# Performance work log

Hardware: AMD Instinct MI355X
Metric: run time of the kernel (lower is better)

## Reference

```python
import jax, jax.numpy as jnp
import numpy as np

N_NODES = 100000
N_EDGES = 1000000
IN_FEAT = 128
OUT_FEAT = 128
NUM_RELS = 64
NUM_BASES = 16
SUBMAT_IN = IN_FEAT // NUM_BASES   # 8
SUBMAT_OUT = OUT_FEAT // NUM_BASES # 8


def setup_inputs() -> dict:
    key = jax.random.key(0)
    k = jax.random.split(key, 8)
    h = jax.random.normal(k[0], (N_NODES, IN_FEAT), dtype=jnp.float32)
    norm = jax.random.uniform(k[1], (N_EDGES, 1), dtype=jnp.float32)
    src = jax.random.randint(k[2], (N_EDGES,), 0, N_NODES, dtype=jnp.int32)
    dst = jax.random.randint(k[3], (N_EDGES,), 0, N_NODES, dtype=jnp.int32)
    r = jax.random.randint(k[4], (N_EDGES,), 0, NUM_RELS, dtype=jnp.int32)
    # learned params (xavier-uniform style scale)
    wscale = np.sqrt(6.0 / (SUBMAT_IN + SUBMAT_OUT)) * np.sqrt(2.0)
    weight = jax.random.uniform(k[5], (NUM_RELS, NUM_BASES * SUBMAT_IN * SUBMAT_OUT),
                                minval=-wscale, maxval=wscale, dtype=jnp.float32)
    lscale = np.sqrt(6.0 / (IN_FEAT + OUT_FEAT)) * np.sqrt(2.0)
    loop_weight = jax.random.uniform(k[6], (IN_FEAT, OUT_FEAT),
                                     minval=-lscale, maxval=lscale, dtype=jnp.float32)
    h_bias = jnp.zeros((OUT_FEAT,), dtype=jnp.float32)
    return {"h": h, "norm": norm, "weight": weight, "loop_weight": loop_weight,
            "h_bias": h_bias, "src": src, "dst": dst, "r": r}


def reference(h, norm, weight, loop_weight, h_bias, src, dst, r):
    E = src.shape[0]
    # per-edge block-diagonal weights: (E, B, si, so)
    w = weight[r].reshape(E, NUM_BASES, SUBMAT_IN, SUBMAT_OUT)
    # src features split into blocks: (E, B, si)
    hs = h[src].reshape(E, NUM_BASES, SUBMAT_IN)
    # small bmm per block, flatten to (E, OUT_FEAT)
    msg = jnp.einsum('ebi,ebio->ebo', hs, w).reshape(E, OUT_FEAT)
    msg = msg * norm
    # scatter-sum to destination nodes
    agg = jax.ops.segment_sum(msg, dst, num_segments=N_NODES)
    # self-loop message (dropout=0.0) + bias
    out = agg + h_bias + h @ loop_weight
    return jax.nn.relu(out)
```

## Files before the change

### kernel.cpp

```cpp
#include <hip/hip_runtime.h>
#include <stdint.h>

#define N_NODES 100000
#define N_EDGES 1000000
#define IN_F 128
#define OUT_F 128
#define NUM_RELS 64
#define NB_SCAN ((N_NODES + 255) / 256)
#define N_WAVES 16384
#define GEMM_B ((N_NODES + 127) / 128)
#define GATHER_B 256

typedef _Float16 half2v __attribute__((ext_vector_type(2)));

__device__ __forceinline__ float dot2f(uint32_t hu, uint32_t wu, float acc) {
#if __has_builtin(__builtin_amdgcn_fdot2)
    return __builtin_amdgcn_fdot2(__builtin_bit_cast(half2v, hu),
                                  __builtin_bit_cast(half2v, wu), acc, false);
#else
    half2v a = __builtin_bit_cast(half2v, hu);
    half2v b = __builtin_bit_cast(half2v, wu);
    acc = fmaf((float)a.x, (float)b.x, acc);
    acc = fmaf((float)a.y, (float)b.y, acc);
    return acc;
#endif
}

__device__ __forceinline__ uint32_t pkh2(float x, float y) {
    half2v v;
    v.x = (_Float16)x;
    v.y = (_Float16)y;
    return __builtin_bit_cast(uint32_t, v);
}

__global__ __launch_bounds__(256) void prep_gemm_fused(
    const float* __restrict__ h, const float* __restrict__ W,
    const float* __restrict__ bias, float* __restrict__ out,
    const float* __restrict__ weight, uint32_t* __restrict__ wsw,
    const int* __restrict__ dst, int* __restrict__ cnt,
    uint4* __restrict__ h16_4, int n_edges, int do_h16)
{
    if (blockIdx.x < GEMM_B) {
        const int tid = threadIdx.x;
        const int ty = tid >> 4, tx = tid & 15;
        const int node0 = blockIdx.x * 128 + ty * 8;
        const int o0 = tx * 8;

        float acc[8][8];
#pragma unroll
        for (int j = 0; j < 8; ++j)
#pragma unroll
            for (int i = 0; i < 8; ++i) acc[j][i] = 0.f;

        int nidx[8];
#pragma unroll
        for (int j = 0; j < 8; ++j) {
            int n = node0 + j;
            nidx[j] = n < N_NODES ? n : (N_NODES - 1);
        }

        for (int k = 0; k < IN_F; k += 4) {
            float hsv[8][4];
#pragma unroll
            for (int j = 0; j < 8; ++j) {
                float4 hv = *reinterpret_cast<const float4*>(h + (size_t)nidx[j] * IN_F + k);
                *reinterpret_cast<float4*>(hsv[j]) = hv;
            }
#pragma unroll
            for (int kk = 0; kk < 4; ++kk) {
                const float* wrow = W + (size_t)(k + kk) * OUT_F + o0;
                float wr[8];
                *reinterpret_cast<float4*>(wr)     = *reinterpret_cast<const float4*>(wrow);
                *reinterpret_cast<float4*>(wr + 4) = *reinterpret_cast<const float4*>(wrow + 4);
#pragma unroll
                for (int j = 0; j < 8; ++j) {
                    const float hk = hsv[j][kk];
#pragma unroll
                    for (int i = 0; i < 8; ++i)
                        acc[j][i] = fmaf(hk, wr[i], acc[j][i]);
                }
            }
        }

        float br[8];
        *reinterpret_cast<float4*>(br)     = *reinterpret_cast<const float4*>(bias + o0);
        *reinterpret_cast<float4*>(br + 4) = *reinterpret_cast<const float4*>(bias + o0 + 4);

#pragma unroll
        for (int j = 0; j < 8; ++j) {
            int n = node0 + j;
            if (n < N_NODES) {
                float4 v0, v1;
                v0.x = acc[j][0] + br[0]; v0.y = acc[j][1] + br[1];
                v0.z = acc[j][2] + br[2]; v0.w = acc[j][3] + br[3];
                v1.x = acc[j][4] + br[4]; v1.y = acc[j][5] + br[5];
                v1.z = acc[j][6] + br[6]; v1.w = acc[j][7] + br[7];
                float* op = out + (size_t)n * OUT_F + o0;
                *reinterpret_cast<float4*>(op)     = v0;
                *reinterpret_cast<float4*>(op + 4) = v1;
            }
        }
        return;
    }

    int t = (blockIdx.x - GEMM_B) * 256 + threadIdx.x;
    if (t < NUM_RELS * 512) {
        int r    = t >> 9;
        int p    = t & 511;
        int half = p >> 8;
        int w8   = p & 255;
        int l    = w8 >> 2;
        int ip   = w8 & 3;
        int b    = l >> 2;
        int q    = l & 3;
        int o    = 2 * q + half;
        const float* s = weight + (size_t)r * 1024 + b * 64 + (2 * ip) * 8 + o;
        half2v v;
        v.x = (_Float16)s[0];
        v.y = (_Float16)s[8];
        wsw[t] = __builtin_bit_cast(uint32_t, v);
        return;
    }
    int e = t - NUM_RELS * 512;
    if (e < n_edges) {
        atomicAdd(&cnt[dst[e]], 1);
        return;
    }
    if (!do_h16) return;
    int t2 = e - n_edges;
    if (t2 < N_NODES * IN_F / 8) {
        const float4* hp = reinterpret_cast<const float4*>(h + (size_t)t2 * 8);
        float4 a = hp[0], c = hp[1];
        uint4 r;
        r.x = pkh2(a.x, a.y);
        r.y = pkh2(a.z, a.w);
        r.z = pkh2(c.x, c.y);
        r.w = pkh2(c.z, c.w);
        h16_4[t2] = r;
    }
}

__global__ __launch_bounds__(256) void block_sums(
    const int* __restrict__ cnt, int* __restrict__ part, int n)
{
    __shared__ int sdata[256];
    int i = blockIdx.x * 256 + threadIdx.x;
    sdata[threadIdx.x] = (i < n) ? cnt[i] : 0;
    __syncthreads();
    for (int s = 128; s > 0; s >>= 1) {
        if (threadIdx.x < s) sdata[threadIdx.x] += sdata[threadIdx.x + s];
        __syncthreads();
    }
    if (threadIdx.x == 0) part[blockIdx.x] = sdata[0];
}

__global__ __launch_bounds__(256) void write_off2(
    const int* __restrict__ cnt, const int* __restrict__ part,
    int* __restrict__ off, int* __restrict__ cur, int n, int n_edges)
{
    __shared__ int sdata[256];
    __shared__ int buf[256];
    const int tid = threadIdx.x;
    const int bid = blockIdx.x;

    int psum = 0;
    for (int t = tid; t < bid; t += 256) psum += part[t];
    sdata[tid] = psum;
    __syncthreads();
    for (int s = 128; s > 0; s >>= 1) {
        if (tid < s) sdata[tid] += sdata[tid + s];
        __syncthreads();
    }
    const int blockoff = sdata[0];

    int i = bid * 256 + tid;
    int v = (i < n) ? cnt[i] : 0;
    buf[tid] = v;
    __syncthreads();
    for (int ofs = 1; ofs < 256; ofs <<= 1) {
        int t = (tid >= ofs) ? buf[tid - ofs] : 0;
        __syncthreads();
        buf[tid] += t;
        __syncthreads();
    }
    int excl = buf[tid] - v + blockoff;
    if (i < n) { off[i] = excl; cur[i] = excl; }
    if (i == n - 1) off[n] = n_edges;
}

__global__ __launch_bounds__(256) void fill_and_part(
    const int* __restrict__ src, const int* __restrict__ dst,
    const int* __restrict__ rel, const float* __restrict__ norm,
    int* __restrict__ cur, int2* __restrict__ emeta,
    const int* __restrict__ off, int* __restrict__ wstart, int n_edges)
{
    int t = blockIdx.x * 256 + threadIdx.x;
    if (t < n_edges) {
        int d = dst[t];
        int p = atomicAdd(&cur[d], 1);
        int2 m;
        m.x = src[t] | (rel[t] << 20);
        m.y = __float_as_int(norm[t]);
        emeta[p] = m;
    } else {
        int w = t - n_edges;
        if (w <= N_WAVES) {
            if (w == 0) {
                wstart[0] = 0;
            } else if (w == N_WAVES) {
                wstart[N_WAVES] = N_NODES;
            } else {
                int target = (int)(((long long)N_EDGES * w) / N_WAVES);
                int lo = 0, hi = N_NODES - 1;
                while (lo < hi) {
                    int mid = (lo + hi) >> 1;
                    if (off[mid + 1] > target) hi = mid; else lo = mid + 1;
                }
                wstart[w] = lo;
            }
        } else if (w <= N_WAVES + 3) {
            int2 z; z.x = 0; z.y = 0;
            emeta[n_edges + (w - N_WAVES - 1)] = z;
        }
    }
}

__global__ __launch_bounds__(1024, 4) void gather_nodes10(
    const uint4* __restrict__ h16_4, const uint32_t* __restrict__ wsw,
    const int* __restrict__ off, const int2* __restrict__ emeta,
    const int* __restrict__ wstart, float* __restrict__ out)
{
    __shared__ uint32_t wlds[NUM_RELS * 512];

    {
        uint4* l4 = reinterpret_cast<uint4*>(wlds);
        const uint4* g4 = reinterpret_cast<const uint4*>(wsw);
        int t = threadIdx.x;
#pragma unroll
        for (int k = 0; k < 8; ++k)
            l4[t + k * 1024] = g4[t + k * 1024];
    }
    __syncthreads();

    const int lane = threadIdx.x & 63;
    const int wid  = threadIdx.x >> 6;
    const int b = lane >> 2;
    const int q = lane & 3;
    const uint32_t lbase = (uint32_t)(lane * 4);

    for (int wv = blockIdx.x * 16 + wid; wv < N_WAVES; wv += GATHER_B * 16) {
        const int n0 = wstart[wv];
        const int n1 = wstart[wv + 1];
        if (n0 >= n1) continue;

        int j = off[n0];
        int e_next = off[n0 + 1];

        int2 m0 = emeta[j];
        int2 m1 = emeta[j + 1];
        int2 m2 = emeta[j + 2];
        uint4 hv0 = h16_4[((uint32_t)m0.x & 0xFFFFFu) * 16 + b];
        uint4 hv1 = h16_4[((uint32_t)m1.x & 0xFFFFFu) * 16 + b];

        uint32_t base0 = ((uint32_t)m0.x >> 20) * 512 + lbase;
        uint4 wa = *reinterpret_cast<const uint4*>(&wlds[base0]);
        uint4 wb = *reinterpret_cast<const uint4*>(&wlds[base0 + 256]);

        for (int d = n0; d < n1; ++d) {
            const int idx2 = (d + 2 < n1) ? d + 2 : n1;
            const int e_nn = off[idx2];
            float a0 = 0.f, a1 = 0.f;

            while (j < e_next) {
                int2 m3 = emeta[j + 3];
                uint4 hv2 = h16_4[((uint32_t)m2.x & 0xFFFFFu) * 16 + b];
                uint32_t bn = ((uint32_t)m1.x >> 20) * 512 + lbase;
                uint4 wna = *reinterpret_cast<const uint4*>(&wlds[bn]);
                uint4 wnb = *reinterpret_cast<const uint4*>(&wlds[bn + 256]);

                float s0 = dot2f(hv0.x, wa.x, 0.f);
                s0 = dot2f(hv0.y, wa.y, s0);
                s0 = dot2f(hv0.z, wa.z, s0);
                s0 = dot2f(hv0.w, wa.w, s0);
                float s1 = dot2f(hv0.x, wb.x, 0.f);
                s1 = dot2f(hv0.y, wb.y, s1);
                s1 = dot2f(hv0.z, wb.z, s1);
                s1 = dot2f(hv0.w, wb.w, s1);

                const float nm = __int_as_float(m0.y);
                a0 = fmaf(s0, nm, a0);
                a1 = fmaf(s1, nm, a1);

                m0 = m1; m1 = m2; m2 = m3;
                hv0 = hv1; hv1 = hv2;
                wa = wna; wb = wnb;
                ++j;
            }

            float2* op = reinterpret_cast<float2*>(out + (size_t)d * OUT_F + b * 8 + 2 * q);
            float2 bse = *op;
            float2 res;
            res.x = fmaxf(bse.x + a0, 0.f);
            res.y = fmaxf(bse.y + a1, 0.f);
            *op = res;

            e_next = e_nn;
        }
    }
}

__global__ __launch_bounds__(1024, 4) void gather_nodes6(
    const float* __restrict__ h, const uint32_t* __restrict__ wsw,
    const int* __restrict__ off, const int2* __restrict__ emeta,
    const int* __restrict__ wstart, float* __restrict__ out)
{
    __shared__ uint32_t wlds[NUM_RELS * 512];
    {
        uint4* l4 = reinterpret_cast<uint4*>(wlds);
        const uint4* g4 = reinterpret_cast<const uint4*>(wsw);
        int t = threadIdx.x;
#pragma unroll
        for (int k = 0; k < 8; ++k)
            l4[t + k * 1024] = g4[t + k * 1024];
    }
    __syncthreads();

    const int lane = threadIdx.x & 63;
    const int wid  = threadIdx.x >> 6;
    const int b = lane >> 2;
    const int q = lane & 3;
    const uint32_t lbase = (uint32_t)(lane * 4);

    for (int wv = blockIdx.x * 16 + wid; wv < N_WAVES; wv += GATHER_B * 16) {
        const int n0 = wstart[wv];
        const int n1 = wstart[wv + 1];
        if (n0 >= n1) continue;

        int j = off[n0];
        int2 m0 = emeta[j];
        int2 m1 = emeta[j + 1];
        int2 m2 = emeta[j + 2];

        const float4* hr0 = reinterpret_cast<const float4*>(
            h + (size_t)((uint32_t)m0.x & 0xFFFFFu) * IN_F + b * 8);
        float4 h0A = hr0[0], h0B = hr0[1];
        const float4* hr1 = reinterpret_cast<const float4*>(
            h + (size_t)((uint32_t)m1.x & 0xFFFFFu) * IN_F + b * 8);
        float4 h1A = hr1[0], h1B = hr1[1];

        uint32_t base0 = ((uint32_t)m0.x >> 20) * 512 + lbase;
        uint4 wa = *reinterpret_cast<const uint4*>(&wlds[base0]);
        uint4 wb = *reinterpret_cast<const uint4*>(&wlds[base0 + 256]);

        for (int d = n0; d < n1; ++d) {
            const int end_d = off[d + 1];
            float a0 = 0.f, a1 = 0.f;

            while (j < end_d) {
                int2 m3 = emeta[j + 3];
                const float4* hr2 = reinterpret_cast<const float4*>(
                    h + (size_t)((uint32_t)m2.x & 0xFFFFFu) * IN_F + b * 8);
                float4 h2A = hr2[0], h2B = hr2[1];
                uint32_t bn = ((uint32_t)m1.x >> 20) * 512 + lbase;
                uint4 wna = *reinterpret_cast<const uint4*>(&wlds[bn]);
                uint4 wnb = *reinterpret_cast<const uint4*>(&wlds[bn + 256]);

                uint32_t h01 = __builtin_bit_cast(uint32_t, __builtin_amdgcn_cvt_pkrtz(h0A.x, h0A.y));
                uint32_t h23 = __builtin_bit_cast(uint32_t, __builtin_amdgcn_cvt_pkrtz(h0A.z, h0A.w));
                uint32_t h45 = __builtin_bit_cast(uint32_t, __builtin_amdgcn_cvt_pkrtz(h0B.x, h0B.y));
                uint32_t h67 = __builtin_bit_cast(uint32_t, __builtin_amdgcn_cvt_pkrtz(h0B.z, h0B.w));

                float s0 = dot2f(h01, wa.x, 0.f);
                s0 = dot2f(h23, wa.y, s0);
                s0 = dot2f(h45, wa.z, s0);
                s0 = dot2f(h67, wa.w, s0);
                float s1 = dot2f(h01, wb.x, 0.f);
                s1 = dot2f(h23, wb.y, s1);
                s1 = dot2f(h45, wb.z, s1);
                s1 = dot2f(h67, wb.w, s1);

                const float nm = __int_as_float(m0.y);
                a0 = fmaf(s0, nm, a0);
                a1 = fmaf(s1, nm, a1);

                m0 = m1; m1 = m2; m2 = m3;
                h0A = h1A; h0B = h1B; h1A = h2A; h1B = h2B;
                wa = wna; wb = wnb;
                ++j;
            }

            float2* op = reinterpret_cast<float2*>(out + (size_t)d * OUT_F + b * 8 + 2 * q);
            float2 bse = *op;
            float2 res;
            res.x = fmaxf(bse.x + a0, 0.f);
            res.y = fmaxf(bse.y + a1, 0.f);
            *op = res;
        }
    }
}

extern "C" void kernel_launch(void* const* d_in, const int* in_sizes, int n_in,
                              void* d_out, int out_size, void* d_ws, size_t ws_size,
                              hipStream_t stream)
{
    const float* h      = (const float*)d_in[0];
    const float* norm   = (const float*)d_in[1];
    const float* weight = (const float*)d_in[2];
    const float* loop_w = (const float*)d_in[3];
    const float* bias   = (const float*)d_in[4];
    const int*   src    = (const int*)d_in[5];
    const int*   dst    = (const int*)d_in[6];
    const int*   rel    = (const int*)d_in[7];
    float* out = (float*)d_out;

    char* wsb = (char*)d_ws;
    char* ws0 = wsb;
    int*  cnt    = (int*)wsb;  wsb += sizeof(int) * N_NODES;
    int*  off    = (int*)wsb;  wsb += sizeof(int) * (N_NODES + 1);
    int*  cur    = (int*)wsb;  wsb += sizeof(int) * N_NODES;
    int*  part   = (int*)wsb;  wsb += sizeof(int) * 512;
    int*  wstart = (int*)wsb;  wsb += sizeof(int) * (N_WAVES + 1);
    wsb = (char*)(((uintptr_t)wsb + 15) & ~(uintptr_t)15);
    uint32_t* wsw = (uint32_t*)wsb; wsb += sizeof(uint32_t) * NUM_RELS * 512;
    int2* emeta = (int2*)wsb;  wsb += sizeof(int2) * (N_EDGES + 3);
    wsb = (char*)(((uintptr_t)wsb + 15) & ~(uintptr_t)15);
    uint4* h16_4 = (uint4*)wsb; wsb += (size_t)N_NODES * IN_F * 2;

    const int use_h16 = (size_t)(wsb - ws0) <= ws_size;

    hipMemsetAsync(cnt, 0, sizeof(int) * N_NODES, stream);

    const int h16_threads = use_h16 ? (N_NODES * IN_F / 8) : 0;
    const int prep_blocks = (NUM_RELS * 512 + N_EDGES + h16_threads + 255) / 256;
    prep_gemm_fused<<<GEMM_B + prep_blocks, 256, 0, stream>>>(
        h, loop_w, bias, out, weight, wsw, dst, cnt, h16_4, N_EDGES, use_h16);
    block_sums<<<NB_SCAN, 256, 0, stream>>>(cnt, part, N_NODES);
    write_off2<<<NB_SCAN, 256, 0, stream>>>(cnt, part, off, cur, N_NODES, N_EDGES);
    const int fp_grid = (N_EDGES + N_WAVES + 4 + 255) / 256;
    fill_and_part<<<fp_grid, 256, 0, stream>>>(src, dst, rel, norm, cur, emeta,
                                               off, wstart, N_EDGES);

    if (use_h16) {
        gather_nodes10<<<GATHER_B, 1024, 0, stream>>>(h16_4, wsw, off, emeta, wstart, out);
    } else {
        gather_nodes6<<<GATHER_B, 1024, 0, stream>>>(h, wsw, off, emeta, wstart, out);
    }
}
```

Measured before the change: 309.5 us.

## Split GEMM from histogram prep and fuse fp16 conversion into GEMM tiles

Splits the combined prep kernel in two. A small kernel now does the weight swizzle and the destination histogram, and a separate GEMM kernel runs after the CSR build. The GEMM kernel also writes the fp16 copy of h for the rows it has just read, so that conversion can reuse data likely still in cache instead of reading h a second time. The trade-off is an extra launch, and the GEMM no longer overlaps with the histogram atomics.

Result: slower. 320.5 us (+3.6%).

```diff
diff --git a/kernel.cpp b/kernel.cpp
--- a/kernel.cpp
+++ b/kernel.cpp
@@ -8,8 +8,9 @@
 #define NUM_RELS 64
 #define NB_SCAN ((N_NODES + 255) / 256)
 #define N_WAVES 16384
-#define GEMM_B ((N_NODES + 127) / 128)
 #define GATHER_B 256
+#define GEMM_TILES ((N_NODES + 127) / 128)
+#define H16_ITEMS (N_NODES * IN_F / 8)
 
 typedef _Float16 half2v __attribute__((ext_vector_type(2)));
 
@@ -33,111 +34,123 @@
     return __builtin_bit_cast(uint32_t, v);
 }
 
-__global__ __launch_bounds__(256) void prep_gemm_fused(
+__device__ __forceinline__ void wsw_write_one(
+    const float* __restrict__ weight, uint32_t* __restrict__ wsw, int t)
+{
+    int r    = t >> 9;
+    int p    = t & 511;
+    int half = p >> 8;
+    int w8   = p & 255;
+    int l    = w8 >> 2;
+    int ip   = w8 & 3;
+    int b    = l >> 2;
+    int q    = l & 3;
+    int o    = 2 * q + half;
+    const float* s = weight + (size_t)r * 1024 + b * 64 + (2 * ip) * 8 + o;
+    half2v v;
+    v.x = (_Float16)s[0];
+    v.y = (_Float16)s[8];
+    wsw[t] = __builtin_bit_cast(uint32_t, v);
+}
+
+__global__ __launch_bounds__(256) void gemm_h16(
     const float* __restrict__ h, const float* __restrict__ W,
     const float* __restrict__ bias, float* __restrict__ out,
+    uint4* __restrict__ h16_4, int do_h16)
+{
+    const int tid = threadIdx.x;
+    const int ty = tid >> 4, tx = tid & 15;
+    const int node0 = blockIdx.x * 128 + ty * 8;
+    const int o0 = tx * 8;
+
+    float acc[8][8];
+#pragma unroll
+    for (int j = 0; j < 8; ++j)
+#pragma unroll
+        for (int i = 0; i < 8; ++i) acc[j][i] = 0.f;
+
+    int nidx[8];
+#pragma unroll
+    for (int j = 0; j < 8; ++j) {
+        int n = node0 + j;
+        nidx[j] = n < N_NODES ? n : (N_NODES - 1);
+    }
+
+    for (int k = 0; k < IN_F; k += 4) {
+        float hsv[8][4];
+#pragma unroll
+        for (int j = 0; j < 8; ++j) {
+            float4 hv = *reinterpret_cast<const float4*>(h + (size_t)nidx[j] * IN_F + k);
+            *reinterpret_cast<float4*>(hsv[j]) = hv;
+        }
+#pragma unroll
+        for (int kk = 0; kk < 4; ++kk) {
+            const float* wrow = W + (size_t)(k + kk) * OUT_F + o0;
+            float wr[8];
+            *reinterpret_cast<float4*>(wr)     = *reinterpret_cast<const float4*>(wrow);
+            *reinterpret_cast<float4*>(wr + 4) = *reinterpret_cast<const float4*>(wrow + 4);
+#pragma unroll
+            for (int j = 0; j < 8; ++j) {
+                const float hk = hsv[j][kk];
+#pragma unroll
+                for (int i = 0; i < 8; ++i)
+                    acc[j][i] = fmaf(hk, wr[i], acc[j][i]);
+            }
+        }
+    }
+
+    float br[8];
+    *reinterpret_cast<float4*>(br)     = *reinterpret_cast<const float4*>(bias + o0);
+    *reinterpret_cast<float4*>(br + 4) = *reinterpret_cast<const float4*>(bias + o0 + 4);
+
+#pragma unroll
+    for (int j = 0; j < 8; ++j) {
+        int n = node0 + j;
+        if (n < N_NODES) {
+            float4 v0, v1;
+            v0.x = acc[j][0] + br[0]; v0.y = acc[j][1] + br[1];
+            v0.z = acc[j][2] + br[2]; v0.w = acc[j][3] + br[3];
+            v1.x = acc[j][4] + br[4]; v1.y = acc[j][5] + br[5];
+            v1.z = acc[j][6] + br[6]; v1.w = acc[j][7] + br[7];
+            float* op = out + (size_t)n * OUT_F + o0;
+            *reinterpret_cast<float4*>(op)     = v0;
+            *reinterpret_cast<float4*>(op + 4) = v1;
+        }
+    }
+
+    if (do_h16) {
+        int node = blockIdx.x * 128 + (tid >> 1);
+        if (node < N_NODES) {
+            const int c0 = (tid & 1) * 64;
+            const float4* hp = reinterpret_cast<const float4*>(
+                h + (size_t)node * IN_F + c0);
+            uint4* dst4 = h16_4 + (size_t)node * 16 + (tid & 1) * 8;
+#pragma unroll
+            for (int k = 0; k < 8; ++k) {
+                float4 a = hp[2 * k];
+                float4 c = hp[2 * k + 1];
+                uint4 r;
+                r.x = pkh2(a.x, a.y);
+                r.y = pkh2(a.z, a.w);
+                r.z = pkh2(c.x, c.y);
+                r.w = pkh2(c.z, c.w);
+                dst4[k] = r;
+            }
+        }
+    }
+}
+
+__global__ __launch_bounds__(256) void hist_wsw(
     const float* __restrict__ weight, uint32_t* __restrict__ wsw,
-    const int* __restrict__ dst, int* __restrict__ cnt,
-    uint4* __restrict__ h16_4, int n_edges, int do_h16)
-{
-    if (blockIdx.x < GEMM_B) {
-        const int tid = threadIdx.x;
-        const int ty = tid >> 4, tx = tid & 15;
-        const int node0 = blockIdx.x * 128 + ty * 8;
-        const int o0 = tx * 8;
-
-        float acc[8][8];
-#pragma unroll
-        for (int j = 0; j < 8; ++j)
-#pragma unroll
-            for (int i = 0; i < 8; ++i) acc[j][i] = 0.f;
-
-        int nidx[8];
-#pragma unroll
-        for (int j = 0; j < 8; ++j) {
-            int n = node0 + j;
-            nidx[j] = n < N_NODES ? n : (N_NODES - 1);
-        }
-
-        for (int k = 0; k < IN_F; k += 4) {
-            float hsv[8][4];
-#pragma unroll
-            for (int j = 0; j < 8; ++j) {
-                float4 hv = *reinterpret_cast<const float4*>(h + (size_t)nidx[j] * IN_F + k);
-                *reinterpret_cast<float4*>(hsv[j]) = hv;
-            }
-#pragma unroll
-            for (int kk = 0; kk < 4; ++kk) {
-                const float* wrow = W + (size_t)(k + kk) * OUT_F + o0;
-                float wr[8];
-                *reinterpret_cast<float4*>(wr)     = *reinterpret_cast<const float4*>(wrow);
-                *reinterpret_cast<float4*>(wr + 4) = *reinterpret_cast<const float4*>(wrow + 4);
-#pragma unroll
-                for (int j = 0; j < 8; ++j) {
-                    const float hk = hsv[j][kk];
-#pragma unroll
-                    for (int i = 0; i < 8; ++i)
-                        acc[j][i] = fmaf(hk, wr[i], acc[j][i]);
-                }
-            }
-        }
-
-        float br[8];
-        *reinterpret_cast<float4*>(br)     = *reinterpret_cast<const float4*>(bias + o0);
-        *reinterpret_cast<float4*>(br + 4) = *reinterpret_cast<const float4*>(bias + o0 + 4);
-
-#pragma unroll
-        for (int j = 0; j < 8; ++j) {
-            int n = node0 + j;
-            if (n < N_NODES) {
-                float4 v0, v1;
-                v0.x = acc[j][0] + br[0]; v0.y = acc[j][1] + br[1];
-                v0.z = acc[j][2] + br[2]; v0.w = acc[j][3] + br[3];
-                v1.x = acc[j][4] + br[4]; v1.y = acc[j][5] + br[5];
-                v1.z = acc[j][6] + br[6]; v1.w = acc[j][7] + br[7];
-                float* op = out + (size_t)n * OUT_F + o0;
-                *reinterpret_cast<float4*>(op)     = v0;
-                *reinterpret_cast<float4*>(op + 4) = v1;
-            }
-        }
+    const int* __restrict__ dst, int* __restrict__ cnt, int n_edges)
+{
+    int t = blockIdx.x * 256 + threadIdx.x;
+    if (t < NUM_RELS * 512) {
+        wsw_write_one(weight, wsw, t);
         return;
     }
-
-    int t = (blockIdx.x - GEMM_B) * 256 + threadIdx.x;
-    if (t < NUM_RELS * 512) {
-        int r    = t >> 9;
-        int p    = t & 511;
-        int half = p >> 8;
-        int w8   = p & 255;
-        int l    = w8 >> 2;
-        int ip   = w8 & 3;
-        int b    = l >> 2;
-        int q    = l & 3;
-        int o    = 2 * q + half;
-        const float* s = weight + (size_t)r * 1024 + b * 64 + (2 * ip) * 8 + o;
-        half2v v;
-        v.x = (_Float16)s[0];
-        v.y = (_Float16)s[8];
-        wsw[t] = __builtin_bit_cast(uint32_t, v);
-        return;
-    }
     int e = t - NUM_RELS * 512;
-    if (e < n_edges) {
-        atomicAdd(&cnt[dst[e]], 1);
-        return;
-    }
-    if (!do_h16) return;
-    int t2 = e - n_edges;
-    if (t2 < N_NODES * IN_F / 8) {
-        const float4* hp = reinterpret_cast<const float4*>(h + (size_t)t2 * 8);
-        float4 a = hp[0], c = hp[1];
-        uint4 r;
-        r.x = pkh2(a.x, a.y);
-        r.y = pkh2(a.z, a.w);
-        r.z = pkh2(c.x, c.y);
-        r.w = pkh2(c.z, c.w);
-        h16_4[t2] = r;
-    }
+    if (e < n_edges) atomicAdd(&cnt[dst[e]], 1);
 }
 
 __global__ __launch_bounds__(256) void block_sums(
@@ -231,7 +244,6 @@
     const int* __restrict__ wstart, float* __restrict__ out)
 {
     __shared__ uint32_t wlds[NUM_RELS * 512];
-
     {
         uint4* l4 = reinterpret_cast<uint4*>(wlds);
         const uint4* g4 = reinterpret_cast<const uint4*>(wsw);
@@ -430,16 +442,16 @@
 
     hipMemsetAsync(cnt, 0, sizeof(int) * N_NODES, stream);
 
-    const int h16_threads = use_h16 ? (N_NODES * IN_F / 8) : 0;
-    const int prep_blocks = (NUM_RELS * 512 + N_EDGES + h16_threads + 255) / 256;
-    prep_gemm_fused<<<GEMM_B + prep_blocks, 256, 0, stream>>>(
-        h, loop_w, bias, out, weight, wsw, dst, cnt, h16_4, N_EDGES, use_h16);
+    const int hw_grid = (NUM_RELS * 512 + N_EDGES + 255) / 256;
+    hist_wsw<<<hw_grid, 256, 0, stream>>>(weight, wsw, dst, cnt, N_EDGES);
     block_sums<<<NB_SCAN, 256, 0, stream>>>(cnt, part, N_NODES);
     write_off2<<<NB_SCAN, 256, 0, stream>>>(cnt, part, off, cur, N_NODES, N_EDGES);
     const int fp_grid = (N_EDGES + N_WAVES + 4 + 255) / 256;
     fill_and_part<<<fp_grid, 256, 0, stream>>>(src, dst, rel, norm, cur, emeta,
                                                off, wstart, N_EDGES);
 
+    gemm_h16<<<GEMM_TILES, 256, 0, stream>>>(h, loop_w, bias, out, h16_4, use_h16);
+
     if (use_h16) {
         gather_nodes10<<<GATHER_B, 1024, 0, stream>>>(h16_4, wsw, off, emeta, wstart, out);
     } else {
```
